# Performance work log

Measured on AMD Instinct MI355X. Metric: run time of the kernel, lower is better.

## Reference

```python
import jax, jax.numpy as jnp
import numpy as np

B = 1024          # batch
N = 48            # NUM_NOTES
OCT = 12          # OCTAVE
NOCT = 4          # NUM_OCTAVES
TU = 256          # TIME_AXIS_UNITS
NU = 128          # NOTE_AXIS_UNITS
IN_T = 1 + OCT + (2 * OCT + 1) + OCT  # 50, time-axis LSTM input
IN_N = TU + 1                          # 257, note-axis LSTM input


def setup_inputs() -> dict:
    key = jax.random.key(0)
    ks = jax.random.split(key, 16)
    s = 0.05
    w = lambda k, shape: jax.random.normal(k, shape, jnp.float32) * s
    return dict(
        note_input=(jax.random.uniform(ks[0], (B, N)) < 0.1).astype(jnp.float32),
        targets=(jax.random.uniform(ks[1], (B, N)) < 0.1).astype(jnp.float32),
        # TimeAxis 2-layer LSTM (b = b_ih + b_hh fused, mathematically identical)
        t_Wih0=w(ks[2], (4 * TU, IN_T)), t_Whh0=w(ks[3], (4 * TU, TU)), t_b0=w(ks[4], (4 * TU,)),
        t_Wih1=w(ks[5], (4 * TU, TU)), t_Whh1=w(ks[6], (4 * TU, TU)), t_b1=w(ks[7], (4 * TU,)),
        # NoteAxis 2-layer LSTM
        n_Wih0=w(ks[8], (4 * NU, IN_N)), n_Whh0=w(ks[9], (4 * NU, NU)), n_b0=w(ks[10], (4 * NU,)),
        n_Wih1=w(ks[11], (4 * NU, NU)), n_Whh1=w(ks[12], (4 * NU, NU)), n_b1=w(ks[13], (4 * NU,)),
        out_W=w(ks[14], (1, NU)), out_b=w(ks[15], (1,)),
    )


def lstm_cell(x, h, c, Wih, Whh, b):
    # PyTorch LSTM gate order: i, f, g, o
    g = x @ Wih.T + h @ Whh.T + b
    i, f, gg, o = jnp.split(g, 4, axis=-1)
    c = jax.nn.sigmoid(f) * c + jax.nn.sigmoid(i) * jnp.tanh(gg)
    h = jax.nn.sigmoid(o) * jnp.tanh(c)
    return h, c


def reference(note_input, targets,
              t_Wih0, t_Whh0, t_b0, t_Wih1, t_Whh1, t_b1,
              n_Wih0, n_Whh0, n_b0, n_Wih1, n_Whh1, n_b1,
              out_W, out_b):
    # ---- TimeAxis (states=None => every note is an independent single LSTM step) ----
    pitch_pos = jnp.arange(N, dtype=jnp.float32) / N                      # [N]
    pitch_class = jnp.tile(jnp.eye(OCT, dtype=jnp.float32), (NOCT, 1))    # [N, OCT]
    chord = note_input.reshape(B, OCT, NOCT).sum(-1)                      # [B, OCT]
    xp = jnp.pad(note_input, ((0, 0), (OCT, OCT)))                        # [B, N+2*OCT]
    vic_idx = jnp.arange(N)[:, None] + jnp.arange(2 * OCT + 1)[None, :]   # [N, 25]
    vicinity = xp[:, vic_idx]                                             # [B, N, 25]
    rnn_in = jnp.concatenate([
        jnp.broadcast_to(pitch_pos[None, :, None], (B, N, 1)),
        jnp.broadcast_to(pitch_class[None], (B, N, OCT)),
        vicinity,
        jnp.broadcast_to(chord[:, None, :], (B, N, OCT)),
    ], axis=-1).reshape(B * N, IN_T)
    z = jnp.zeros((B * N, TU), rnn_in.dtype)
    h1, _ = lstm_cell(rnn_in, z, z, t_Wih0, t_Whh0, t_b0)
    h2, _ = lstm_cell(h1, z, z, t_Wih1, t_Whh1, t_b1)
    feats = h2.reshape(B, N, TU)                                          # [B, N, TU]

    # ---- NoteAxis (teacher-forced sequential LSTM over notes) ----
    cond = jnp.concatenate([jnp.zeros((B, 1), feats.dtype), targets[:, :-1]], axis=1)  # [B, N]
    xs = jnp.concatenate([feats, cond[..., None]], axis=-1).transpose(1, 0, 2)  # [N, B, IN_N]
    z1 = jnp.zeros((B, NU), feats.dtype)

    def step(carry, x):
        h1, c1, h2, c2 = carry
        h1, c1 = lstm_cell(x, h1, c1, n_Wih0, n_Whh0, n_b0)
        h2, c2 = lstm_cell(h1, h2, c2, n_Wih1, n_Whh1, n_b1)
        return (h1, c1, h2, c2), h2

    _, hs = jax.lax.scan(step, (z1, z1, z1, z1), xs)                      # [N, B, NU]
    out = jax.nn.sigmoid(jnp.einsum('nbh,oh->bno', hs, out_W) + out_b)    # [B, N, 1]
    return out[..., 0]
```

## Files before the change

### kernel.cpp

```cpp
#include <hip/hip_runtime.h>

typedef unsigned short ushort_t;
typedef unsigned int uint_t;
typedef _Float16 f16_t;
typedef _Float16 half8_t __attribute__((ext_vector_type(8)));
typedef float floatx4 __attribute__((ext_vector_type(4)));
typedef unsigned int uintx4 __attribute__((ext_vector_type(4)));

#define LOG2E 1.44269504088896f
#define TWO_LOG2E 2.88539008177793f

__device__ __forceinline__ ushort_t f2h_bits(float f) {
    f16_t h = (f16_t)f;
    return __builtin_bit_cast(ushort_t, h);
}
__device__ __forceinline__ float h2f(ushort_t u) {
    return (float)__builtin_bit_cast(f16_t, u);
}
__device__ __forceinline__ float h2f_lo(uint_t u) { return h2f((ushort_t)(u & 0xFFFF)); }
__device__ __forceinline__ float h2f_hi(uint_t u) { return h2f((ushort_t)(u >> 16)); }

__device__ __forceinline__ float sigm2(float x) {
    return __builtin_amdgcn_rcpf(1.0f + __builtin_amdgcn_exp2f(-x));
}
__device__ __forceinline__ float tanh2(float y) {
    return __builtin_fmaf(-2.0f, __builtin_amdgcn_rcpf(1.0f + __builtin_amdgcn_exp2f(y)), 1.0f);
}
__device__ __forceinline__ float tanhc(float c) {
    return tanh2(c * TWO_LOG2E);
}

__device__ __forceinline__ half8_t ldfrag(const ushort_t* p, int V, int kt, int q, int n) {
    return *(const half8_t*)(p + ((size_t)((kt * 4 + q) * V + n)) * 8);
}

__device__ __forceinline__ void pack_one(
    const float* srcA, int KA, const float* srcB, int KB,
    ushort_t* dst, int V, int K, int idx)
{
    int v = idx / K, k = idx - v * K;
    float val = 0.0f;
    if (k < KA) val = srcA[v * KA + k];
    else if (k < KA + KB) val = srcB[v * KB + (k - KA)];
    float sc = ((v >> 7) == 2) ? TWO_LOG2E : LOG2E;
    int kt = k >> 5, qq = (k >> 3) & 3, j = k & 7;
    dst[((size_t)((kt * 4 + qq) * V + v)) * 8 + j] = f2h_bits(val * sc);
}

__device__ __forceinline__ void pack_tl_one(
    const float* src, int Ksrc, ushort_t* dst, int K, int idx)
{
    int v = idx / K, k = idx - v * K;
    int r = (v < 256) ? v : v + 256;
    float val = (k < Ksrc) ? src[r * Ksrc + k] : 0.0f;
    float sc = (v >= 256 && v < 512) ? TWO_LOG2E : LOG2E;
    int kt = k >> 5, qq = (k >> 3) & 3, j = k & 7;
    dst[((size_t)((kt * 4 + qq) * 768 + v)) * 8 + j] = f2h_bits(val * sc);
}

__global__ __launch_bounds__(256) void packAll(
    const float* __restrict__ tWih0, const float* __restrict__ tWih1,
    const float* __restrict__ nWih0, const float* __restrict__ nWhh0,
    const float* __restrict__ nWih1, const float* __restrict__ nWhh1,
    ushort_t* __restrict__ W0m, ushort_t* __restrict__ W1m,
    ushort_t* __restrict__ N0x, ushort_t* __restrict__ N0m,
    ushort_t* __restrict__ N1m)
{
    int idx = blockIdx.x * 256 + threadIdx.x;
    if (idx < 49152) { pack_tl_one(tWih0, 50, W0m, 64, idx); return; }
    idx -= 49152;
    if (idx < 196608) { pack_tl_one(tWih1, 256, W1m, 256, idx); return; }
    idx -= 196608;
    if (idx < 131072) { pack_one(nWih0, 257, (const float*)0, 0, N0x, 512, 256, idx); return; }
    idx -= 131072;
    if (idx < 65536) { pack_one(nWhh0, 128, (const float*)0, 0, N0m, 512, 128, idx); return; }
    idx -= 65536;
    if (idx < 131072) { pack_one(nWih1, 128, nWhh1, 128, N1m, 512, 256, idx); return; }
}

__global__ __launch_bounds__(512, 6) void fusedA(
    const float* __restrict__ note, const float* __restrict__ targets,
    const ushort_t* __restrict__ W0m, const float* __restrict__ b0,
    const ushort_t* __restrict__ W1m, const float* __restrict__ b1,
    const ushort_t* __restrict__ N0x, const float* __restrict__ nWih0raw,
    const float* __restrict__ nb0,
    uint_t* __restrict__ G1u)
{
    __shared__ __align__(16) ushort_t xAa[32 * 64];
    __shared__ __align__(16) ushort_t xH1[32 * 256];
    __shared__ __align__(16) ushort_t xH2[32 * 256];
    const int tid = threadIdx.x;
    const int wv = tid >> 6, l = tid & 63, l16 = l & 15, q = l >> 4;
    const int r0A = blockIdx.x * 32;

    for (int idx = tid; idx < 32 * 64; idx += 512) {
        int r = idx >> 6, c = idx & 63;
        int row = r0A + r;
        int b = row / 48, n = row - b * 48;
        float val = 0.0f;
        if (c == 0) val = (float)n * (1.0f / 48.0f);
        else if (c < 13) val = ((n % 12) == (c - 1)) ? 1.0f : 0.0f;
        else if (c < 38) {
            int p = n + (c - 13) - 12;
            if (p >= 0 && p < 48) val = note[b * 48 + p];
        } else if (c < 50) {
            const float* nb = note + b * 48 + (c - 38) * 4;
            val = nb[0] + nb[1] + nb[2] + nb[3];
        }
        int kb = c >> 3, j = c & 7;
        xAa[r * 64 + (((kb ^ r) & 7) << 3) + j] = f2h_bits(val);
    }
    __syncthreads();

#pragma unroll
    for (int s = 0; s < 2; ++s) {
        const int u = (wv * 2 + s) * 16 + l16;
        floatx4 acc[2][3] = {};
#pragma unroll
        for (int kt = 0; kt < 2; ++kt) {
            half8_t bI = ldfrag(W0m, 768, kt, q, u);
            half8_t bG = ldfrag(W0m, 768, kt, q, 256 + u);
            half8_t bO = ldfrag(W0m, 768, kt, q, 512 + u);
            int kbp = ((kt * 4 + q) ^ l16) & 7;
#pragma unroll
            for (int mt = 0; mt < 2; ++mt) {
                half8_t a = *(const half8_t*)&xAa[(mt * 16 + l16) * 64 + kbp * 8];
                acc[mt][0] = __builtin_amdgcn_mfma_f32_16x16x32_f16(a, bI, acc[mt][0], 0, 0, 0);
                acc[mt][1] = __builtin_amdgcn_mfma_f32_16x16x32_f16(a, bG, acc[mt][1], 0, 0, 0);
                acc[mt][2] = __builtin_amdgcn_mfma_f32_16x16x32_f16(a, bO, acc[mt][2], 0, 0, 0);
            }
        }
        float bi = b0[u] * LOG2E, bg = b0[512 + u] * TWO_LOG2E, bo = b0[768 + u] * LOG2E;
        int kbW = u >> 3;
#pragma unroll
        for (int mt = 0; mt < 2; ++mt)
#pragma unroll
            for (int r = 0; r < 4; ++r) {
                float c = sigm2(acc[mt][0][r] + bi) * tanh2(acc[mt][1][r] + bg);
                float h = sigm2(acc[mt][2][r] + bo) * tanhc(c);
                int m = mt * 16 + q * 4 + r;
                int kbp = (kbW & 16) | ((kbW ^ (m & 15)) & 15);
                xH1[m * 256 + kbp * 8 + (u & 7)] = f2h_bits(h);
            }
    }
    __syncthreads();

#pragma unroll
    for (int s = 0; s < 2; ++s) {
        const int u = (wv * 2 + s) * 16 + l16;
        floatx4 acc[2][3] = {};
#pragma unroll
        for (int kt = 0; kt < 8; ++kt) {
            half8_t bI = ldfrag(W1m, 768, kt, q, u);
            half8_t bG = ldfrag(W1m, 768, kt, q, 256 + u);
            half8_t bO = ldfrag(W1m, 768, kt, q, 512 + u);
            int kb = kt * 4 + q;
            int kbp = (kb & 16) | ((kb ^ l16) & 15);
#pragma unroll
            for (int mt = 0; mt < 2; ++mt) {
                half8_t a = *(const half8_t*)&xH1[(mt * 16 + l16) * 256 + kbp * 8];
                acc[mt][0] = __builtin_amdgcn_mfma_f32_16x16x32_f16(a, bI, acc[mt][0], 0, 0, 0);
                acc[mt][1] = __builtin_amdgcn_mfma_f32_16x16x32_f16(a, bG, acc[mt][1], 0, 0, 0);
                acc[mt][2] = __builtin_amdgcn_mfma_f32_16x16x32_f16(a, bO, acc[mt][2], 0, 0, 0);
            }
        }
        float bi = b1[u] * LOG2E, bg = b1[512 + u] * TWO_LOG2E, bo = b1[768 + u] * LOG2E;
        int kbW = u >> 3;
#pragma unroll
        for (int mt = 0; mt < 2; ++mt)
#pragma unroll
            for (int r = 0; r < 4; ++r) {
                float c = sigm2(acc[mt][0][r] + bi) * tanh2(acc[mt][1][r] + bg);
                float h = sigm2(acc[mt][2][r] + bo) * tanhc(c);
                int m = mt * 16 + q * 4 + r;
                int kbp = (kbW & 16) | ((kbW ^ (m & 15)) & 15);
                xH2[m * 256 + kbp * 8 + (u & 7)] = f2h_bits(h);
            }
    }
    __syncthreads();

    {
        const int u2 = wv * 16 + l16;
        floatx4 acc[2][4] = {};
#pragma unroll
        for (int kt = 0; kt < 8; ++kt) {
            half8_t bf[4];
#pragma unroll
            for (int g = 0; g < 4; ++g) bf[g] = ldfrag(N0x, 512, kt, q, g * 128 + u2);
            int kb = kt * 4 + q;
            int kbp = (kb & 16) | ((kb ^ l16) & 15);
#pragma unroll
            for (int mt = 0; mt < 2; ++mt) {
                half8_t a = *(const half8_t*)&xH2[(mt * 16 + l16) * 256 + kbp * 8];
#pragma unroll
                for (int g = 0; g < 4; ++g)
                    acc[mt][g] = __builtin_amdgcn_mfma_f32_16x16x32_f16(a, bf[g], acc[mt][g], 0, 0, 0);
            }
        }
        float bias[4], wc[4];
#pragma unroll
        for (int g = 0; g < 4; ++g) {
            float sc = (g == 2) ? TWO_LOG2E : LOG2E;
            bias[g] = nb0[g * 128 + u2] * sc;
            wc[g] = nWih0raw[(size_t)(g * 128 + u2) * 257 + 256] * sc;
        }
#pragma unroll
        for (int mt = 0; mt < 2; ++mt) {
#pragma unroll
            for (int r = 0; r < 4; ++r) {
                int R = r0A + mt * 16 + q * 4 + r;
                int b = R / 48;
                int t = R - b * 48;
                float cond = (t > 0) ? targets[R - 1] : 0.0f;
                float vi = acc[mt][0][r] + bias[0] + cond * wc[0];
                float vf = acc[mt][1][r] + bias[1] + cond * wc[1];
                float vg = acc[mt][2][r] + bias[2] + cond * wc[2];
                float vo = acc[mt][3][r] + bias[3] + cond * wc[3];
                uint_t lo = (uint_t)f2h_bits(vi) | ((uint_t)f2h_bits(vf) << 16);
                uint_t hi = (uint_t)f2h_bits(vg) | ((uint_t)f2h_bits(vo) << 16);
                size_t a = ((size_t)(b >> 4) * 48 + t) * 4096 + (b & 15) * 256 + u2 * 2;
                *(uint2*)(G1u + a) = make_uint2(lo, hi);
            }
        }
    }
}

__global__ __launch_bounds__(512) __attribute__((amdgpu_waves_per_eu(2, 2)))
void phaseB(
    const uint_t* __restrict__ G1u, const ushort_t* __restrict__ N0m,
    const ushort_t* __restrict__ N1m, const float* __restrict__ nb1,
    const float* __restrict__ outW, const float* __restrict__ outb,
    float* __restrict__ out)
{
    __shared__ __align__(16) ushort_t w1s[16 * 512 * 8];
    __shared__ __align__(16) ushort_t xA[16 * 512];
    __shared__ __align__(16) ushort_t owfs[128];
    const int tid = threadIdx.x;
    const int wv = tid >> 6, l = tid & 63, l16 = l & 15, q = l >> 4;
    const int r0 = blockIdx.x * 16;
    const int u = wv * 16 + l16;

    for (int i = tid; i < 8192; i += 512) ((uint4*)w1s)[i] = ((const uint4*)N0m)[i];
    for (int i = tid; i < 1024; i += 512) ((uint4*)xA)[i] = make_uint4(0, 0, 0, 0);
    if (tid < 16) {
        int base = (tid >> 2) * 32 + (tid & 3) * 8;
#pragma unroll
        for (int j = 0; j < 8; ++j)
            owfs[tid * 8 + j] = f2h_bits(outW[base + j] * LOG2E);
    }

    uintx4 B2[8][4];
#pragma unroll
    for (int kt = 0; kt < 8; ++kt)
#pragma unroll
        for (int g = 0; g < 4; ++g)
            B2[kt][g] = *(const uintx4*)(N1m + ((size_t)((kt * 4 + q) * 512 + g * 128 + u)) * 8);

    const float bI = nb1[u] * LOG2E, bF = nb1[128 + u] * LOG2E;
    const float bG = nb1[256 + u] * TWO_LOG2E, bO = nb1[384 + u] * LOG2E;
    const float obs = outb[0] * LOG2E;
    float c1[4], c2[4] = {0, 0, 0, 0};

    const uint_t* g1base = G1u + (size_t)blockIdx.x * 48 * 4096;
    uint2 g1c[4];
#pragma unroll
    for (int r = 0; r < 4; ++r)
        g1c[r] = *(const uint2*)(g1base + (q * 4 + r) * 256 + u * 2);

    const int kbW = u >> 3;
    const int jW = u & 7;

    __syncthreads();

#pragma unroll
    for (int r = 0; r < 4; ++r) {
        float gi = h2f_lo(g1c[r].x);
        float gg = h2f_lo(g1c[r].y);
        float go = h2f_hi(g1c[r].y);
        c1[r] = sigm2(gi) * tanh2(gg);
        float h1v = sigm2(go) * tanhc(c1[r]);
        int m = q * 4 + r;
        xA[m * 512 + (((kbW ^ m) & 15) << 3) + jW] = f2h_bits(h1v);
    }
#pragma unroll
    for (int r = 0; r < 4; ++r)
        g1c[r] = *(const uint2*)(g1base + 4096 + (q * 4 + r) * 256 + u * 2);
    __syncthreads();

    for (int t = 0; t < 48; ++t) {
#pragma unroll
        for (int kt = 0; kt < 8; ++kt)
#pragma unroll
            for (int g = 0; g < 4; ++g)
                asm volatile("" : "+v"(B2[kt][g]));

        const int c = (t & 1) * 128;
        const int pv = c ^ 128;

        half8_t a1[4], a2[4];
#pragma unroll
        for (int kt = 0; kt < 4; ++kt) {
            int kb = kt * 4 + q;
            int kbp = (kb ^ l16) & 15;
            a1[kt] = *(const half8_t*)&xA[l16 * 512 + c + kbp * 8];
            a2[kt] = *(const half8_t*)&xA[l16 * 512 + 256 + pv + kbp * 8];
        }

        floatx4 acc1[4] = {};
#pragma unroll
        for (int kt = 0; kt < 4; ++kt) {
            int kb = kt * 4 + q;
#pragma unroll
            for (int g = 0; g < 4; ++g) {
                half8_t bfr = *(const half8_t*)&w1s[((size_t)(kb * 512 + g * 128 + u)) * 8];
                acc1[g] = __builtin_amdgcn_mfma_f32_16x16x32_f16(a1[kt], bfr, acc1[g], 0, 0, 0);
            }
        }

        floatx4 acc2[4] = {};
        floatx4 accH = {0.0f, 0.0f, 0.0f, 0.0f};
#pragma unroll
        for (int kt = 0; kt < 4; ++kt) {
#pragma unroll
            for (int g = 0; g < 4; ++g)
                acc2[g] = __builtin_amdgcn_mfma_f32_16x16x32_f16(
                    a2[kt], __builtin_bit_cast(half8_t, B2[kt + 4][g]), acc2[g], 0, 0, 0);
            half8_t of = *(const half8_t*)&owfs[(kt * 4 + q) * 8];
            accH = __builtin_amdgcn_mfma_f32_16x16x32_f16(a2[kt], of, accH, 0, 0, 0);
        }
#pragma unroll
        for (int kt = 0; kt < 4; ++kt)
#pragma unroll
            for (int g = 0; g < 4; ++g)
                acc2[g] = __builtin_amdgcn_mfma_f32_16x16x32_f16(
                    a1[kt], __builtin_bit_cast(half8_t, B2[kt][g]), acc2[g], 0, 0, 0);

        if (t > 0 && wv == 0 && l16 == 0) {
#pragma unroll
            for (int r = 0; r < 4; ++r)
                out[(r0 + q * 4 + r) * 48 + (t - 1)] = sigm2(accH[r] + obs);
        }

#pragma unroll
        for (int r = 0; r < 4; ++r) {
            float gi = acc2[0][r] + bI;
            float gf = acc2[1][r] + bF;
            float gg = acc2[2][r] + bG;
            float go = acc2[3][r] + bO;
            c2[r] = sigm2(gf) * c2[r] + sigm2(gi) * tanh2(gg);
            float h2v = sigm2(go) * tanhc(c2[r]);
            int m = q * 4 + r;
            xA[m * 512 + 256 + c + (((kbW ^ m) & 15) << 3) + jW] = f2h_bits(h2v);
        }

        if (t < 47) {
#pragma unroll
            for (int r = 0; r < 4; ++r) {
                float gi = acc1[0][r] + h2f_lo(g1c[r].x);
                float gf = acc1[1][r] + h2f_hi(g1c[r].x);
                float gg = acc1[2][r] + h2f_lo(g1c[r].y);
                float go = acc1[3][r] + h2f_hi(g1c[r].y);
                c1[r] = sigm2(gf) * c1[r] + sigm2(gi) * tanh2(gg);
                float h1v = sigm2(go) * tanhc(c1[r]);
                int m = q * 4 + r;
                xA[m * 512 + pv + (((kbW ^ m) & 15) << 3) + jW] = f2h_bits(h1v);
            }
        }

        {
            int tn = (t < 46) ? t + 2 : 47;
            const uint_t* gp = g1base + (size_t)tn * 4096;
#pragma unroll
            for (int r = 0; r < 4; ++r)
                g1c[r] = *(const uint2*)(gp + (q * 4 + r) * 256 + u * 2);
        }
        __syncthreads();
    }

    {
        floatx4 accH = {0.0f, 0.0f, 0.0f, 0.0f};
#pragma unroll
        for (int kt = 0; kt < 4; ++kt) {
            int kb = kt * 4 + q;
            int kbp = (kb ^ l16) & 15;
            half8_t a2e = *(const half8_t*)&xA[l16 * 512 + 256 + 128 + kbp * 8];
            half8_t of = *(const half8_t*)&owfs[(kt * 4 + q) * 8];
            accH = __builtin_amdgcn_mfma_f32_16x16x32_f16(a2e, of, accH, 0, 0, 0);
        }
        if (wv == 0 && l16 == 0) {
#pragma unroll
            for (int r = 0; r < 4; ++r)
                out[(r0 + q * 4 + r) * 48 + 47] = sigm2(accH[r] + obs);
        }
    }
}

extern "C" void kernel_launch(void* const* d_in, const int* in_sizes, int n_in,
                              void* d_out, int out_size, void* d_ws, size_t ws_size,
                              hipStream_t stream)
{
    const float* note  = (const float*)d_in[0];
    const float* targ  = (const float*)d_in[1];
    const float* tWih0 = (const float*)d_in[2];
    const float* tb0   = (const float*)d_in[4];
    const float* tWih1 = (const float*)d_in[5];
    const float* tb1   = (const float*)d_in[7];
    const float* nWih0 = (const float*)d_in[8];
    const float* nWhh0 = (const float*)d_in[9];
    const float* nb0   = (const float*)d_in[10];
    const float* nWih1 = (const float*)d_in[11];
    const float* nWhh1 = (const float*)d_in[12];
    const float* nb1   = (const float*)d_in[13];
    const float* outW  = (const float*)d_in[14];
    const float* outb  = (const float*)d_in[15];

    char* ws = (char*)d_ws;
    uint_t*   G1u = (uint_t*)(ws);
    ushort_t* W0m = (ushort_t*)(ws + 50331648);
    ushort_t* W1m = (ushort_t*)(ws + 50429952);
    ushort_t* N0x = (ushort_t*)(ws + 50823168);
    ushort_t* N0m = (ushort_t*)(ws + 51085312);
    ushort_t* N1m = (ushort_t*)(ws + 51216384);

    packAll<<<2240, 256, 0, stream>>>(tWih0, tWih1, nWih0, nWhh0, nWih1, nWhh1,
                                      W0m, W1m, N0x, N0m, N1m);
    fusedA<<<1536, 512, 0, stream>>>(note, targ, W0m, tb0, W1m, tb1, N0x, nWih0, nb0, G1u);
    phaseB<<<64, 512, 0, stream>>>(G1u, N0m, N1m, nb1, outW, outb, (float*)d_out);
}
```

Before: 269.6 us.

## Stagger layer-1/layer-2 work order across waves to overlap MFMA and transcendental phases

Each wave is given a role. Half the waves compute the layer-2 MFMAs and elementwise update first and then layer 1, while the other half do the reverse. Waves sharing a SIMD therefore run MFMA and transcendental-heavy elementwise phases at different times, which is meant to raise utilisation of both units in the serial recurrence. The output-projection MFMA is also restricted to wave 0 instead of being computed redundantly by every wave. The cost is a divergent code path per role and extra registers for the double-buffered G1 prefetch.

```diff
diff --git a/kernel.cpp b/kernel.cpp
--- a/kernel.cpp
+++ b/kernel.cpp
@@ -225,6 +225,57 @@
     }
 }
 
+#define MFMA_L1(ACC, A1) do { \
+    _Pragma("unroll") for (int kt = 0; kt < 4; ++kt) { \
+        int kb = kt * 4 + q; \
+        _Pragma("unroll") for (int g = 0; g < 4; ++g) { \
+            half8_t bfr = *(const half8_t*)&w1s[((size_t)(kb * 512 + g * 128 + u)) * 8]; \
+            ACC[g] = __builtin_amdgcn_mfma_f32_16x16x32_f16(A1[kt], bfr, ACC[g], 0, 0, 0); \
+        } } } while (0)
+
+#define MFMA_L2(ACC, A1, A2) do { \
+    _Pragma("unroll") for (int kt = 0; kt < 4; ++kt) \
+        _Pragma("unroll") for (int g = 0; g < 4; ++g) \
+            ACC[g] = __builtin_amdgcn_mfma_f32_16x16x32_f16( \
+                A2[kt], __builtin_bit_cast(half8_t, B2[kt + 4][g]), ACC[g], 0, 0, 0); \
+    _Pragma("unroll") for (int kt = 0; kt < 4; ++kt) \
+        _Pragma("unroll") for (int g = 0; g < 4; ++g) \
+            ACC[g] = __builtin_amdgcn_mfma_f32_16x16x32_f16( \
+                A1[kt], __builtin_bit_cast(half8_t, B2[kt][g]), ACC[g], 0, 0, 0); \
+    } while (0)
+
+#define DO_E2(ACC) do { \
+    _Pragma("unroll") for (int r = 0; r < 4; ++r) { \
+        float gi = ACC[0][r] + bI; \
+        float gf = ACC[1][r] + bF; \
+        float gg = ACC[2][r] + bG; \
+        float go = ACC[3][r] + bO; \
+        c2[r] = sigm2(gf) * c2[r] + sigm2(gi) * tanh2(gg); \
+        float h2v = sigm2(go) * tanhc(c2[r]); \
+        int m = q * 4 + r; \
+        xA[m * 512 + 256 + c + (((kbW ^ m) & 15) << 3) + jW] = f2h_bits(h2v); \
+    } } while (0)
+
+#define DO_E1(ACC, GS) do { \
+    if (t < 47) { \
+        _Pragma("unroll") for (int r = 0; r < 4; ++r) { \
+            float gi = ACC[0][r] + h2f_lo(GS[r].x); \
+            float gf = ACC[1][r] + h2f_hi(GS[r].x); \
+            float gg = ACC[2][r] + h2f_lo(GS[r].y); \
+            float go = ACC[3][r] + h2f_hi(GS[r].y); \
+            c1[r] = sigm2(gf) * c1[r] + sigm2(gi) * tanh2(gg); \
+            float h1v = sigm2(go) * tanhc(c1[r]); \
+            int m = q * 4 + r; \
+            xA[m * 512 + pv + (((kbW ^ m) & 15) << 3) + jW] = f2h_bits(h1v); \
+        } } } while (0)
+
+#define PREF_G1(DST) do { \
+    int tn = (t < 46) ? t + 2 : 47; \
+    const uint_t* gp = g1base + (size_t)tn * 4096; \
+    _Pragma("unroll") for (int r = 0; r < 4; ++r) \
+        DST[r] = *(const uint2*)(gp + (q * 4 + r) * 256 + u * 2); \
+    } while (0)
+
 __global__ __launch_bounds__(512) __attribute__((amdgpu_waves_per_eu(2, 2)))
 void phaseB(
     const uint_t* __restrict__ G1u, const ushort_t* __restrict__ N0m,
@@ -237,6 +288,7 @@
     __shared__ __align__(16) ushort_t owfs[128];
     const int tid = threadIdx.x;
     const int wv = tid >> 6, l = tid & 63, l16 = l & 15, q = l >> 4;
+    const int role = (wv ^ (wv >> 2)) & 1;
     const int r0 = blockIdx.x * 16;
     const int u = wv * 16 + l16;
 
@@ -262,7 +314,7 @@
     float c1[4], c2[4] = {0, 0, 0, 0};
 
     const uint_t* g1base = G1u + (size_t)blockIdx.x * 48 * 4096;
-    uint2 g1c[4];
+    uint2 g1c[4], g1x[4];
 #pragma unroll
     for (int r = 0; r < 4; ++r)
         g1c[r] = *(const uint2*)(g1base + (q * 4 + r) * 256 + u * 2);
@@ -306,78 +358,42 @@
             a2[kt] = *(const half8_t*)&xA[l16 * 512 + 256 + pv + kbp * 8];
         }
 
-        floatx4 acc1[4] = {};
-#pragma unroll
-        for (int kt = 0; kt < 4; ++kt) {
-            int kb = kt * 4 + q;
-#pragma unroll
-            for (int g = 0; g < 4; ++g) {
-                half8_t bfr = *(const half8_t*)&w1s[((size_t)(kb * 512 + g * 128 + u)) * 8];
-                acc1[g] = __builtin_amdgcn_mfma_f32_16x16x32_f16(a1[kt], bfr, acc1[g], 0, 0, 0);
-            }
-        }
-
-        floatx4 acc2[4] = {};
-        floatx4 accH = {0.0f, 0.0f, 0.0f, 0.0f};
-#pragma unroll
-        for (int kt = 0; kt < 4; ++kt) {
-#pragma unroll
-            for (int g = 0; g < 4; ++g)
-                acc2[g] = __builtin_amdgcn_mfma_f32_16x16x32_f16(
-                    a2[kt], __builtin_bit_cast(half8_t, B2[kt + 4][g]), acc2[g], 0, 0, 0);
-            half8_t of = *(const half8_t*)&owfs[(kt * 4 + q) * 8];
-            accH = __builtin_amdgcn_mfma_f32_16x16x32_f16(a2[kt], of, accH, 0, 0, 0);
-        }
-#pragma unroll
-        for (int kt = 0; kt < 4; ++kt)
-#pragma unroll
-            for (int g = 0; g < 4; ++g)
-                acc2[g] = __builtin_amdgcn_mfma_f32_16x16x32_f16(
-                    a1[kt], __builtin_bit_cast(half8_t, B2[kt][g]), acc2[g], 0, 0, 0);
-
-        if (t > 0 && wv == 0 && l16 == 0) {
-#pragma unroll
-            for (int r = 0; r < 4; ++r)
-                out[(r0 + q * 4 + r) * 48 + (t - 1)] = sigm2(accH[r] + obs);
-        }
-
-#pragma unroll
-        for (int r = 0; r < 4; ++r) {
-            float gi = acc2[0][r] + bI;
-            float gf = acc2[1][r] + bF;
-            float gg = acc2[2][r] + bG;
-            float go = acc2[3][r] + bO;
-            c2[r] = sigm2(gf) * c2[r] + sigm2(gi) * tanh2(gg);
-            float h2v = sigm2(go) * tanhc(c2[r]);
-            int m = q * 4 + r;
-            xA[m * 512 + 256 + c + (((kbW ^ m) & 15) << 3) + jW] = f2h_bits(h2v);
-        }
-
-        if (t < 47) {
-#pragma unroll
-            for (int r = 0; r < 4; ++r) {
-                float gi = acc1[0][r] + h2f_lo(g1c[r].x);
-                float gf = acc1[1][r] + h2f_hi(g1c[r].x);
-                float gg = acc1[2][r] + h2f_lo(g1c[r].y);
-                float go = acc1[3][r] + h2f_hi(g1c[r].y);
-                c1[r] = sigm2(gf) * c1[r] + sigm2(gi) * tanh2(gg);
-                float h1v = sigm2(go) * tanhc(c1[r]);
-                int m = q * 4 + r;
-                xA[m * 512 + pv + (((kbW ^ m) & 15) << 3) + jW] = f2h_bits(h1v);
-            }
-        }
-
-        {
-            int tn = (t < 46) ? t + 2 : 47;
-            const uint_t* gp = g1base + (size_t)tn * 4096;
-#pragma unroll
-            for (int r = 0; r < 4; ++r)
-                g1c[r] = *(const uint2*)(gp + (q * 4 + r) * 256 + u * 2);
+        if (role == 0) {
+            floatx4 acc2[4] = {};
+            MFMA_L2(acc2, a1, a2);
+            if (wv == 0) {
+                floatx4 accH = {0.0f, 0.0f, 0.0f, 0.0f};
+#pragma unroll
+                for (int kt = 0; kt < 4; ++kt) {
+                    half8_t of = *(const half8_t*)&owfs[(kt * 4 + q) * 8];
+                    accH = __builtin_amdgcn_mfma_f32_16x16x32_f16(a2[kt], of, accH, 0, 0, 0);
+                }
+                if (t > 0 && l16 == 0) {
+#pragma unroll
+                    for (int r = 0; r < 4; ++r)
+                        out[(r0 + q * 4 + r) * 48 + (t - 1)] = sigm2(accH[r] + obs);
+                }
+            }
+            DO_E2(acc2);
+            PREF_G1(g1x);
+            floatx4 acc1[4] = {};
+            MFMA_L1(acc1, a1);
+            DO_E1(acc1, g1c);
+#pragma unroll
+            for (int r = 0; r < 4; ++r) g1c[r] = g1x[r];
+        } else {
+            floatx4 acc1[4] = {};
+            MFMA_L1(acc1, a1);
+            DO_E1(acc1, g1c);
+            PREF_G1(g1c);
+            floatx4 acc2[4] = {};
+            MFMA_L2(acc2, a1, a2);
+            DO_E2(acc2);
         }
         __syncthreads();
     }
 
-    {
+    if (wv == 0) {
         floatx4 accH = {0.0f, 0.0f, 0.0f, 0.0f};
 #pragma unroll
         for (int kt = 0; kt < 4; ++kt) {
@@ -387,7 +403,7 @@
             half8_t of = *(const half8_t*)&owfs[(kt * 4 + q) * 8];
             accH = __builtin_amdgcn_mfma_f32_16x16x32_f16(a2e, of, accH, 0, 0, 0);
         }
-        if (wv == 0 && l16 == 0) {
+        if (l16 == 0) {
 #pragma unroll
             for (int r = 0; r < 4; ++r)
                 out[(r0 + q * 4 + r) * 48 + 47] = sigm2(accH[r] + obs);
```

After: 267.5 us. No clear change (-0.8%).

## Split note-axis LSTM layers across separate waves with 1024-thread blocks

Applied to the files above, without the earlier changes.

The sequential phaseB kernel now launches 1024 threads, with even waves computing layer-0 recurrence and odd waves computing layer-1 plus the output projection, so the two layers run concurrently within each time step. Layer-1 weights are no longer held in registers (128 VGPRs of B2); they are re-read from global memory (hopefully L1/L2 hits) on every step. This shortens each wave's per-step critical path and raises occupancy, at the cost of global weight-load latency inside the recurrent loop.

```diff
diff --git a/kernel.cpp b/kernel.cpp
--- a/kernel.cpp
+++ b/kernel.cpp
@@ -225,7 +225,7 @@
     }
 }
 
-__global__ __launch_bounds__(512) __attribute__((amdgpu_waves_per_eu(2, 2)))
+__global__ __launch_bounds__(1024) __attribute__((amdgpu_waves_per_eu(4)))
 void phaseB(
     const uint_t* __restrict__ G1u, const ushort_t* __restrict__ N0m,
     const ushort_t* __restrict__ N1m, const float* __restrict__ nb1,
@@ -237,147 +237,156 @@
     __shared__ __align__(16) ushort_t owfs[128];
     const int tid = threadIdx.x;
     const int wv = tid >> 6, l = tid & 63, l16 = l & 15, q = l >> 4;
+    const int lay = wv & 1;
     const int r0 = blockIdx.x * 16;
-    const int u = wv * 16 + l16;
-
-    for (int i = tid; i < 8192; i += 512) ((uint4*)w1s)[i] = ((const uint4*)N0m)[i];
-    for (int i = tid; i < 1024; i += 512) ((uint4*)xA)[i] = make_uint4(0, 0, 0, 0);
+    const int u = (wv >> 1) * 16 + l16;
+
+    for (int i = tid; i < 8192; i += 1024) ((uint4*)w1s)[i] = ((const uint4*)N0m)[i];
+    for (int i = tid; i < 1024; i += 1024) ((uint4*)xA)[i] = make_uint4(0, 0, 0, 0);
     if (tid < 16) {
         int base = (tid >> 2) * 32 + (tid & 3) * 8;
 #pragma unroll
         for (int j = 0; j < 8; ++j)
             owfs[tid * 8 + j] = f2h_bits(outW[base + j] * LOG2E);
     }
-
-    uintx4 B2[8][4];
-#pragma unroll
-    for (int kt = 0; kt < 8; ++kt)
-#pragma unroll
-        for (int g = 0; g < 4; ++g)
-            B2[kt][g] = *(const uintx4*)(N1m + ((size_t)((kt * 4 + q) * 512 + g * 128 + u)) * 8);
 
     const float bI = nb1[u] * LOG2E, bF = nb1[128 + u] * LOG2E;
     const float bG = nb1[256 + u] * TWO_LOG2E, bO = nb1[384 + u] * LOG2E;
     const float obs = outb[0] * LOG2E;
-    float c1[4], c2[4] = {0, 0, 0, 0};
+    float c1[4] = {0, 0, 0, 0}, c2[4] = {0, 0, 0, 0};
 
     const uint_t* g1base = G1u + (size_t)blockIdx.x * 48 * 4096;
+    const ushort_t* nbp = N1m + ((size_t)(q * 512) + u) * 8;
     uint2 g1c[4];
-#pragma unroll
-    for (int r = 0; r < 4; ++r)
-        g1c[r] = *(const uint2*)(g1base + (q * 4 + r) * 256 + u * 2);
+    if (!lay) {
+#pragma unroll
+        for (int r = 0; r < 4; ++r)
+            g1c[r] = *(const uint2*)(g1base + (q * 4 + r) * 256 + u * 2);
+    }
 
     const int kbW = u >> 3;
     const int jW = u & 7;
 
     __syncthreads();
 
-#pragma unroll
-    for (int r = 0; r < 4; ++r) {
-        float gi = h2f_lo(g1c[r].x);
-        float gg = h2f_lo(g1c[r].y);
-        float go = h2f_hi(g1c[r].y);
-        c1[r] = sigm2(gi) * tanh2(gg);
-        float h1v = sigm2(go) * tanhc(c1[r]);
-        int m = q * 4 + r;
-        xA[m * 512 + (((kbW ^ m) & 15) << 3) + jW] = f2h_bits(h1v);
-    }
-#pragma unroll
-    for (int r = 0; r < 4; ++r)
-        g1c[r] = *(const uint2*)(g1base + 4096 + (q * 4 + r) * 256 + u * 2);
+    if (!lay) {
+#pragma unroll
+        for (int r = 0; r < 4; ++r) {
+            float gi = h2f_lo(g1c[r].x);
+            float gg = h2f_lo(g1c[r].y);
+            float go = h2f_hi(g1c[r].y);
+            c1[r] = sigm2(gi) * tanh2(gg);
+            float h1v = sigm2(go) * tanhc(c1[r]);
+            int m = q * 4 + r;
+            xA[m * 512 + (((kbW ^ m) & 15) << 3) + jW] = f2h_bits(h1v);
+        }
+#pragma unroll
+        for (int r = 0; r < 4; ++r)
+            g1c[r] = *(const uint2*)(g1base + 4096 + (q * 4 + r) * 256 + u * 2);
+    }
     __syncthreads();
 
     for (int t = 0; t < 48; ++t) {
-#pragma unroll
-        for (int kt = 0; kt < 8; ++kt)
-#pragma unroll
-            for (int g = 0; g < 4; ++g)
-                asm volatile("" : "+v"(B2[kt][g]));
-
         const int c = (t & 1) * 128;
         const int pv = c ^ 128;
 
-        half8_t a1[4], a2[4];
-#pragma unroll
-        for (int kt = 0; kt < 4; ++kt) {
-            int kb = kt * 4 + q;
-            int kbp = (kb ^ l16) & 15;
-            a1[kt] = *(const half8_t*)&xA[l16 * 512 + c + kbp * 8];
-            a2[kt] = *(const half8_t*)&xA[l16 * 512 + 256 + pv + kbp * 8];
-        }
-
-        floatx4 acc1[4] = {};
-#pragma unroll
-        for (int kt = 0; kt < 4; ++kt) {
-            int kb = kt * 4 + q;
-#pragma unroll
-            for (int g = 0; g < 4; ++g) {
-                half8_t bfr = *(const half8_t*)&w1s[((size_t)(kb * 512 + g * 128 + u)) * 8];
-                acc1[g] = __builtin_amdgcn_mfma_f32_16x16x32_f16(a1[kt], bfr, acc1[g], 0, 0, 0);
-            }
-        }
-
-        floatx4 acc2[4] = {};
-        floatx4 accH = {0.0f, 0.0f, 0.0f, 0.0f};
-#pragma unroll
-        for (int kt = 0; kt < 4; ++kt) {
-#pragma unroll
-            for (int g = 0; g < 4; ++g)
-                acc2[g] = __builtin_amdgcn_mfma_f32_16x16x32_f16(
-                    a2[kt], __builtin_bit_cast(half8_t, B2[kt + 4][g]), acc2[g], 0, 0, 0);
-            half8_t of = *(const half8_t*)&owfs[(kt * 4 + q) * 8];
-            accH = __builtin_amdgcn_mfma_f32_16x16x32_f16(a2[kt], of, accH, 0, 0, 0);
-        }
-#pragma unroll
-        for (int kt = 0; kt < 4; ++kt)
-#pragma unroll
-            for (int g = 0; g < 4; ++g)
-                acc2[g] = __builtin_amdgcn_mfma_f32_16x16x32_f16(
-                    a1[kt], __builtin_bit_cast(half8_t, B2[kt][g]), acc2[g], 0, 0, 0);
-
-        if (t > 0 && wv == 0 && l16 == 0) {
-#pragma unroll
-            for (int r = 0; r < 4; ++r)
-                out[(r0 + q * 4 + r) * 48 + (t - 1)] = sigm2(accH[r] + obs);
-        }
-
-#pragma unroll
-        for (int r = 0; r < 4; ++r) {
-            float gi = acc2[0][r] + bI;
-            float gf = acc2[1][r] + bF;
-            float gg = acc2[2][r] + bG;
-            float go = acc2[3][r] + bO;
-            c2[r] = sigm2(gf) * c2[r] + sigm2(gi) * tanh2(gg);
-            float h2v = sigm2(go) * tanhc(c2[r]);
-            int m = q * 4 + r;
-            xA[m * 512 + 256 + c + (((kbW ^ m) & 15) << 3) + jW] = f2h_bits(h2v);
-        }
-
-        if (t < 47) {
+        if (!lay) {
+            half8_t a1[4];
+#pragma unroll
+            for (int kt = 0; kt < 4; ++kt) {
+                int kb = kt * 4 + q;
+                int kbp = (kb ^ l16) & 15;
+                a1[kt] = *(const half8_t*)&xA[l16 * 512 + c + kbp * 8];
+            }
+            floatx4 acc1[4] = {};
+#pragma unroll
+            for (int kt = 0; kt < 4; ++kt) {
+                int kb = kt * 4 + q;
+#pragma unroll
+                for (int g = 0; g < 4; ++g) {
+                    half8_t bfr = *(const half8_t*)&w1s[((size_t)(kb * 512 + g * 128 + u)) * 8];
+                    acc1[g] = __builtin_amdgcn_mfma_f32_16x16x32_f16(a1[kt], bfr, acc1[g], 0, 0, 0);
+                }
+            }
+            if (t < 47) {
+#pragma unroll
+                for (int r = 0; r < 4; ++r) {
+                    float gi = acc1[0][r] + h2f_lo(g1c[r].x);
+                    float gf = acc1[1][r] + h2f_hi(g1c[r].x);
+                    float gg = acc1[2][r] + h2f_lo(g1c[r].y);
+                    float go = acc1[3][r] + h2f_hi(g1c[r].y);
+                    c1[r] = sigm2(gf) * c1[r] + sigm2(gi) * tanh2(gg);
+                    float h1v = sigm2(go) * tanhc(c1[r]);
+                    int m = q * 4 + r;
+                    xA[m * 512 + pv + (((kbW ^ m) & 15) << 3) + jW] = f2h_bits(h1v);
+                }
+            }
+            {
+                int tn = (t < 46) ? t + 2 : 47;
+                const uint_t* gp = g1base + (size_t)tn * 4096;
+#pragma unroll
+                for (int r = 0; r < 4; ++r)
+                    g1c[r] = *(const uint2*)(gp + (q * 4 + r) * 256 + u * 2);
+            }
+        } else {
+            half8_t a1[4], a2[4];
+#pragma unroll
+            for (int kt = 0; kt < 4; ++kt) {
+                int kb = kt * 4 + q;
+                int kbp = (kb ^ l16) & 15;
+                a1[kt] = *(const half8_t*)&xA[l16 * 512 + c + kbp * 8];
+                a2[kt] = *(const half8_t*)&xA[l16 * 512 + 256 + pv + kbp * 8];
+            }
+            floatx4 acc2[4] = {};
+#pragma unroll
+            for (int kt = 4; kt < 8; ++kt) {
+                half8_t bf[4];
+#pragma unroll
+                for (int g = 0; g < 4; ++g)
+                    bf[g] = *(const half8_t*)(nbp + ((size_t)kt * 2048 + g * 128) * 8);
+#pragma unroll
+                for (int g = 0; g < 4; ++g)
+                    acc2[g] = __builtin_amdgcn_mfma_f32_16x16x32_f16(a2[kt - 4], bf[g], acc2[g], 0, 0, 0);
+            }
+            if (wv == 1) {
+                floatx4 accH = {0.0f, 0.0f, 0.0f, 0.0f};
+#pragma unroll
+                for (int kt = 0; kt < 4; ++kt) {
+                    half8_t of = *(const half8_t*)&owfs[(kt * 4 + q) * 8];
+                    accH = __builtin_amdgcn_mfma_f32_16x16x32_f16(a2[kt], of, accH, 0, 0, 0);
+                }
+                if (t > 0 && l16 == 0) {
+#pragma unroll
+                    for (int r = 0; r < 4; ++r)
+                        out[(r0 + q * 4 + r) * 48 + (t - 1)] = sigm2(accH[r] + obs);
+                }
+            }
+#pragma unroll
+            for (int kt = 0; kt < 4; ++kt) {
+                half8_t bf[4];
+#pragma unroll
+                for (int g = 0; g < 4; ++g)
+                    bf[g] = *(const half8_t*)(nbp + ((size_t)kt * 2048 + g * 128) * 8);
+#pragma unroll
+                for (int g = 0; g < 4; ++g)
+                    acc2[g] = __builtin_amdgcn_mfma_f32_16x16x32_f16(a1[kt], bf[g], acc2[g], 0, 0, 0);
+            }
 #pragma unroll
             for (int r = 0; r < 4; ++r) {
-                float gi = acc1[0][r] + h2f_lo(g1c[r].x);
-                float gf = acc1[1][r] + h2f_hi(g1c[r].x);
-                float gg = acc1[2][r] + h2f_lo(g1c[r].y);
-                float go = acc1[3][r] + h2f_hi(g1c[r].y);
-                c1[r] = sigm2(gf) * c1[r] + sigm2(gi) * tanh2(gg);
-                float h1v = sigm2(go) * tanhc(c1[r]);
+                float gi = acc2[0][r] + bI;
+                float gf = acc2[1][r] + bF;
+                float gg = acc2[2][r] + bG;
+                float go = acc2[3][r] + bO;
+                c2[r] = sigm2(gf) * c2[r] + sigm2(gi) * tanh2(gg);
+                float h2v = sigm2(go) * tanhc(c2[r]);
                 int m = q * 4 + r;
-                xA[m * 512 + pv + (((kbW ^ m) & 15) << 3) + jW] = f2h_bits(h1v);
-            }
-        }
-
-        {
-            int tn = (t < 46) ? t + 2 : 47;
-            const uint_t* gp = g1base + (size_t)tn * 4096;
-#pragma unroll
-            for (int r = 0; r < 4; ++r)
-                g1c[r] = *(const uint2*)(gp + (q * 4 + r) * 256 + u * 2);
+                xA[m * 512 + 256 + c + (((kbW ^ m) & 15) << 3) + jW] = f2h_bits(h2v);
+            }
         }
         __syncthreads();
     }
 
-    {
+    if (wv == 1) {
         floatx4 accH = {0.0f, 0.0f, 0.0f, 0.0f};
 #pragma unroll
         for (int kt = 0; kt < 4; ++kt) {
@@ -387,7 +396,7 @@
             half8_t of = *(const half8_t*)&owfs[(kt * 4 + q) * 8];
             accH = __builtin_amdgcn_mfma_f32_16x16x32_f16(a2e, of, accH, 0, 0, 0);
         }
-        if (wv == 0 && l16 == 0) {
+        if (l16 == 0) {
 #pragma unroll
             for (int r = 0; r < 4; ++r)
                 out[(r0 + q * 4 + r) * 48 + 47] = sigm2(accH[r] + obs);
@@ -425,5 +434,5 @@
     packAll<<<2240, 256, 0, stream>>>(tWih0, tWih1, nWih0, nWhh0, nWih1, nWhh1,
                                       W0m, W1m, N0x, N0m, N1m);
     fusedA<<<1536, 512, 0, stream>>>(note, targ, W0m, tb0, W1m, tb1, N0x, nWih0, nb0, G1u);
-    phaseB<<<64, 512, 0, stream>>>(G1u, N0m, N1m, nb1, outW, outb, (float*)d_out);
-}
+    phaseB<<<64, 1024, 0, stream>>>(G1u, N0m, N1m, nb1, outW, outb, (float*)d_out);
+}
```

Result: slower. 455.2 us (+68.9%).
